# Kernel optimization log

Hardware: AMD Instinct MI355X
Metric: run time of the kernel (lower is better)

Reference implementation:

```python
import jax, jax.numpy as jnp
import numpy as np

EMBED_DIM = 1024
NUM_HEADS = 16
EFF_HEADS = NUM_HEADS // 2
HEAD_DIM = EMBED_DIM // NUM_HEADS
LAMBDA_INIT = 0.8
B, N = 2, 2048


def setup_inputs() -> dict:
    key = jax.random.key(0)
    ks = jax.random.split(key, 14)
    s = 0.02
    return {
        "x": jax.random.normal(ks[0], (B, N, EMBED_DIM), dtype=jnp.float32),
        "Wq": jax.random.normal(ks[1], (EMBED_DIM, EMBED_DIM), dtype=jnp.float32) * s,
        "bq": jnp.zeros((EMBED_DIM,), dtype=jnp.float32),
        "Wk": jax.random.normal(ks[2], (EMBED_DIM, EMBED_DIM), dtype=jnp.float32) * s,
        "bk": jnp.zeros((EMBED_DIM,), dtype=jnp.float32),
        "Wv": jax.random.normal(ks[3], (EMBED_DIM, EMBED_DIM), dtype=jnp.float32) * s,
        "bv": jnp.zeros((EMBED_DIM,), dtype=jnp.float32),
        "Wp": jax.random.normal(ks[4], (EMBED_DIM, EMBED_DIM), dtype=jnp.float32) * s,
        "bp": jnp.zeros((EMBED_DIM,), dtype=jnp.float32),
        "lambda_q1": jax.random.normal(ks[5], (EFF_HEADS, 1, HEAD_DIM), dtype=jnp.float32) * s,
        "lambda_k1": jax.random.normal(ks[6], (EFF_HEADS, 1, HEAD_DIM), dtype=jnp.float32) * s,
        "lambda_q2": jax.random.normal(ks[7], (EFF_HEADS, 1, HEAD_DIM), dtype=jnp.float32) * s,
        "lambda_k2": jax.random.normal(ks[8], (EFF_HEADS, 1, HEAD_DIM), dtype=jnp.float32) * s,
    }


def reference(x, Wq, bq, Wk, bk, Wv, bv, Wp, bp,
              lambda_q1, lambda_k1, lambda_q2, lambda_k2):
    Bb, Nn, C = x.shape
    H, H2, hd = NUM_HEADS, EFF_HEADS, HEAD_DIM
    scale = hd ** (-0.5)

    # projections (torch Linear: y = x @ W.T + b), reshape to [B,H,N,hd]
    q = (x @ Wq.T + bq).reshape(Bb, Nn, H, hd).transpose(0, 2, 1, 3)
    k = (x @ Wk.T + bk).reshape(Bb, Nn, H, hd).transpose(0, 2, 1, 3)
    v = (x @ Wv.T + bv).reshape(Bb, Nn, H, hd).transpose(0, 2, 1, 3)

    q1, q2 = q[:, :H2], q[:, H2:]
    k1, k2 = k[:, :H2], k[:, H2:]
    v1, v2 = v[:, :H2], v[:, H2:]

    # scalar lambda: per-head dot products, clamped exp, differenced, averaged
    l1 = jnp.exp(jnp.minimum((lambda_q1 * lambda_k1).sum((-1, -2)), 5.0))  # [H2]
    l2 = jnp.exp(jnp.minimum((lambda_q2 * lambda_k2).sum((-1, -2)), 5.0))
    lv = (l1 - l2 + LAMBDA_INIT).mean()

    a1 = jax.nn.softmax(jnp.einsum('bhnd,bhmd->bhnm', q1, k1) * scale, axis=-1)
    x1 = jnp.einsum('bhnm,bhmd->bhnd', a1, v1).transpose(0, 2, 1, 3).reshape(Bb, Nn, C // 2)
    a2 = jax.nn.softmax(jnp.einsum('bhnd,bhmd->bhnm', q2, k2) * scale, axis=-1)
    x2 = jnp.einsum('bhnm,bhmd->bhnd', a2, v2).transpose(0, 2, 1, 3).reshape(Bb, Nn, C // 2)

    out = jnp.concatenate([x1 - lv * x2, x2], axis=-1) @ Wp.T + bp
    return out
```

## Files before the change

kernel.cpp:

```cpp
#include <hip/hip_runtime.h>

typedef __bf16 bf16;
typedef __bf16 bf16x8 __attribute__((ext_vector_type(8)));
typedef __bf16 bf16x4 __attribute__((ext_vector_type(4)));
typedef float  f32x16 __attribute__((ext_vector_type(16)));
typedef unsigned int uint;
typedef unsigned int uintx4 __attribute__((ext_vector_type(4)));

#define QSCALE (0.125f * 1.44269504088896340736f)

__device__ __forceinline__ void g2l16(const void* g, void* l) {
  __builtin_amdgcn_global_load_lds(
      (const __attribute__((address_space(1))) void*)g,
      (__attribute__((address_space(3))) void*)l, 16, 0, 0);
}

__device__ __forceinline__ f32x16 mfma16(bf16x8 a, bf16x8 b, f32x16 c) {
  return __builtin_amdgcn_mfma_f32_32x32x16_bf16(a, b, c, 0, 0, 0);
}

__global__ void cast5_kernel(const float* __restrict__ x,
                             const float* __restrict__ wq, const float* __restrict__ wk,
                             const float* __restrict__ wv, const float* __restrict__ wp,
                             const float* __restrict__ lq1, const float* __restrict__ lk1,
                             const float* __restrict__ lq2, const float* __restrict__ lk2,
                             bf16* __restrict__ xb, bf16* __restrict__ wqkv,
                             bf16* __restrict__ wpb) {
  int seg = blockIdx.y;
  long i = (long)(blockIdx.x * 256 + threadIdx.x) * 8;
  const float* s; bf16* d; long n;
  if (seg == 0)      { s = x;  d = xb;  n = 4194304; }
  else if (seg == 1) { s = wq; d = wqkv;            n = 1048576; }
  else if (seg == 2) { s = wk; d = wqkv + 1048576;  n = 1048576; }
  else if (seg == 3) { s = wv; d = wqkv + 2097152;  n = 1048576; }
  else               { s = wp; d = wpb;             n = 1048576; }
  if (i >= n) return;
  float4 f0 = *(const float4*)(s + i);
  float4 f1 = *(const float4*)(s + i + 4);
  if (seg == 4 && (i & 1023) >= 512) {
    int t = threadIdx.x & 63;
    float accum = 0.f;
    for (int hh = 0; hh < 8; ++hh) {
      float v1 = lq1[hh*64 + t] * lk1[hh*64 + t];
      float v2 = lq2[hh*64 + t] * lk2[hh*64 + t];
      for (int off = 32; off; off >>= 1) {
        v1 += __shfl_xor(v1, off);
        v2 += __shfl_xor(v2, off);
      }
      accum += expf(fminf(v1, 5.f)) - expf(fminf(v2, 5.f));
    }
    float lv = accum / 8.f + 0.8f;
    float4 g0 = *(const float4*)(s + i - 512);
    float4 g1 = *(const float4*)(s + i - 508);
    f0.x -= lv * g0.x; f0.y -= lv * g0.y; f0.z -= lv * g0.z; f0.w -= lv * g0.w;
    f1.x -= lv * g1.x; f1.y -= lv * g1.y; f1.z -= lv * g1.z; f1.w -= lv * g1.w;
  }
  bf16x8 o;
  o[0] = (bf16)f0.x; o[1] = (bf16)f0.y; o[2] = (bf16)f0.z; o[3] = (bf16)f0.w;
  o[4] = (bf16)f1.x; o[5] = (bf16)f1.y; o[6] = (bf16)f1.z; o[7] = (bf16)f1.w;
  *(bf16x8*)(d + i) = o;
}

__global__ __launch_bounds__(256, 2) void gemm_qkv_kernel(
    const bf16* __restrict__ A, const bf16* __restrict__ B,
    const float* __restrict__ bias0, const float* __restrict__ bias1,
    const float* __restrict__ bias2,
    bf16* __restrict__ O0, bf16* __restrict__ O1, bf16* __restrict__ O2) {
  __shared__ __align__(16) char smem[32 * 1024];
  const int tid = threadIdx.x;
  const int w = tid >> 6, L = tid & 63;
  const int l31 = L & 31, h5 = L >> 5;
  const int m0 = blockIdx.x * 128;
  const int n0g = blockIdx.y * 128;
  const int by = n0g >> 10;
  const bf16* Bp = B + (long)by * 1048576;
  const float* biasp = (by == 0) ? bias0 : ((by == 1) ? bias1 : bias2);
  const int nloc = n0g & 1023;

  f32x16 acc[2][2];
  for (int i = 0; i < 2; ++i) for (int j = 0; j < 2; ++j)
    for (int r = 0; r < 16; ++r) acc[i][j][r] = 0.f;

  const int srow = L >> 1, spar = L & 1;
  const int wm = w >> 1, wn = w & 1;
  const int fs = (l31 * 2 + h5) * 16;

  for (int k0 = 0; k0 < 1024; k0 += 64) {
    for (int i = 0; i < 8; ++i) {
      int r = w * 8 + i;
      int rr = r & 15;
      int rowblk = rr >> 2, kst = rr & 3;
      int row = rowblk * 32 + srow;
      int kk = k0 + (kst * 2 + spar) * 8;
      const bf16* gsrc = (r < 16) ? (A + (long)(m0 + row) * 1024 + kk)
                                  : (Bp + (long)(nloc + row) * 1024 + kk);
      g2l16(gsrc, smem + r * 1024);
    }
    __syncthreads();
    for (int kst = 0; kst < 4; ++kst) {
      bf16x8 a0 = *(const bf16x8*)(smem + (((wm * 2 + 0) * 4 + kst) * 1024) + fs);
      bf16x8 a1 = *(const bf16x8*)(smem + (((wm * 2 + 1) * 4 + kst) * 1024) + fs);
      bf16x8 b0 = *(const bf16x8*)(smem + 16384 + (((wn * 2 + 0) * 4 + kst) * 1024) + fs);
      bf16x8 b1 = *(const bf16x8*)(smem + 16384 + (((wn * 2 + 1) * 4 + kst) * 1024) + fs);
      acc[0][0] = mfma16(a0, b0, acc[0][0]);
      acc[0][1] = mfma16(a0, b1, acc[0][1]);
      acc[1][0] = mfma16(a1, b0, acc[1][0]);
      acc[1][1] = mfma16(a1, b1, acc[1][1]);
    }
    __syncthreads();
  }

  if (by == 2) {
    int b = m0 >> 11;
    int nbase = (m0 & 2047);
    for (int mi = 0; mi < 2; ++mi) for (int ni = 0; ni < 2; ++ni) {
      int col = nloc + wn * 64 + ni * 32 + l31;
      int hh = col >> 6, d = col & 63;
      float bias_v = biasp[col];
      long rowbase = ((long)(b * 16 + hh) * 64 + d) * 2048 + nbase + wm * 64;
      for (int g = 0; g < 4; ++g) {
        bf16x4 pk;
        for (int r = 0; r < 4; ++r) pk[r] = (bf16)(acc[mi][ni][g * 4 + r] + bias_v);
        int Qp = mi * 4 + g;
        int slot = (Qp >> 1) * 16 + h5 * 8 + (Qp & 1) * 4;
        *(bf16x4*)(O2 + rowbase + slot) = pk;
      }
    }
  } else {
    bf16* dst = (by == 0) ? O0 : O1;
    float scale = (by == 0) ? QSCALE : 1.0f;
    for (int mi = 0; mi < 2; ++mi) for (int ni = 0; ni < 2; ++ni) {
      int col = nloc + wn * 64 + ni * 32 + l31;
      float bias_v = biasp[col];
      int row_base = m0 + wm * 64 + mi * 32 + 4 * h5;
      for (int reg = 0; reg < 16; ++reg) {
        int rowoff = (reg & 3) + 8 * (reg >> 2);
        float v = (acc[mi][ni][reg] + bias_v) * scale;
        dst[(long)(row_base + rowoff) * 1024 + col] = (bf16)v;
      }
    }
  }
}

__global__ __launch_bounds__(256, 2) void gemm_proj_kernel(
    const bf16* __restrict__ A, const bf16* __restrict__ B,
    const float* __restrict__ bias, float* __restrict__ Of) {
  __shared__ __align__(16) char smem[24 * 1024];
  const int tid = threadIdx.x;
  const int w = tid >> 6, L = tid & 63;
  const int l31 = L & 31, h5 = L >> 5;
  const int m0 = blockIdx.x * 64;
  const int nloc = blockIdx.y * 128;

  f32x16 acc[2];
  for (int i = 0; i < 2; ++i)
    for (int r = 0; r < 16; ++r) acc[i][r] = 0.f;

  const int srow = L >> 1, spar = L & 1;
  const int fs = (l31 * 2 + h5) * 16;

  for (int k0 = 0; k0 < 1024; k0 += 64) {
    for (int i = 0; i < 6; ++i) {
      int r = w * 6 + i;
      const bf16* gsrc;
      if (r < 8) {
        int rowblk = r >> 2, kst = r & 3;
        gsrc = A + (long)(m0 + rowblk * 32 + srow) * 1024 + k0 + (kst * 2 + spar) * 8;
      } else {
        int rr = r - 8;
        int rowblk = rr >> 2, kst = rr & 3;
        gsrc = B + (long)(nloc + rowblk * 32 + srow) * 1024 + k0 + (kst * 2 + spar) * 8;
      }
      g2l16(gsrc, smem + r * 1024);
    }
    __syncthreads();
    for (int kst = 0; kst < 4; ++kst) {
      bf16x8 a0 = *(const bf16x8*)(smem + ((0 * 4 + kst) * 1024) + fs);
      bf16x8 a1 = *(const bf16x8*)(smem + ((1 * 4 + kst) * 1024) + fs);
      bf16x8 bb = *(const bf16x8*)(smem + 8192 + ((w * 4 + kst) * 1024) + fs);
      acc[0] = mfma16(a0, bb, acc[0]);
      acc[1] = mfma16(a1, bb, acc[1]);
    }
    __syncthreads();
  }

  for (int mi = 0; mi < 2; ++mi) {
    int col = nloc + w * 32 + l31;
    float bias_v = bias[col];
    int row_base = m0 + mi * 32 + 4 * h5;
    for (int reg = 0; reg < 16; ++reg) {
      int rowoff = (reg & 3) + 8 * (reg >> 2);
      Of[(long)(row_base + rowoff) * 1024 + col] = acc[mi][reg] + bias_v;
    }
  }
}

__global__ __launch_bounds__(512, 4) void attn_kernel(
    const bf16* __restrict__ Qb, const bf16* __restrict__ Kb,
    const bf16* __restrict__ Vt, bf16* __restrict__ Ob) {
  __shared__ __align__(16) char smem[65536];
  const int tid = threadIdx.x, w = tid >> 6, L = tid & 63;
  const int half = w >> 2, pair = w & 3;
  const int bh = blockIdx.x, qt = blockIdx.y;
  const int b = bh >> 4, h = bh & 15;
  const int q0 = qt * 128 + pair * 32;
  const int l31 = L & 31, h5 = L >> 5;
  const int srow = L >> 1, spar = L & 1;
  const int fs = (l31 * 2 + h5) * 16;

  bf16x8 qf[4];
  for (int kst = 0; kst < 4; ++kst)
    qf[kst] = *(const bf16x8*)(Qb + (long)(b * 2048 + q0 + l31) * 1024 + h * 64
                               + kst * 16 + h5 * 8);

  f32x16 o[2];
  for (int i = 0; i < 2; ++i)
    for (int r = 0; r < 16; ++r) o[i][r] = 0.f;
  float ls[4] = {0.f, 0.f, 0.f, 0.f};

  const bf16* Kbh = Kb + (long)b * 2048 * 1024 + h * 64 + (long)half * 1024 * 1024;
  const bf16* Vth = Vt + (long)bh * 64 * 2048 + half * 1024;

  char* kb0 = smem + half * 16384;
  char* kb1 = smem + 32768 + half * 16384;

  auto stage = [&](int t, char* kb) {
    int n0 = t * 64;
    for (int i = 0; i < 4; ++i) {
      int r = pair * 4 + i;
      if (r < 8) {
        int nkb = r >> 2, kst = r & 3;
        const bf16* g = Kbh + (long)(n0 + nkb * 32 + srow) * 1024 + (kst * 2 + spar) * 8;
        g2l16(g, kb + r * 1024);
      } else {
        int rr = r - 8, db = rr >> 2, kst = rr & 3;
        const bf16* g = Vth + (long)(db * 32 + srow) * 2048 + n0 + (kst * 2 + spar) * 8;
        g2l16(g, kb + 8192 + rr * 1024);
      }
    }
  };

  stage(0, kb0);
  stage(1, kb1);

  for (int t = 0; t < 16; ++t) {
    char* kb = (t & 1) ? kb1 : kb0;
    if (t < 15) asm volatile("s_waitcnt vmcnt(4)" ::: "memory");
    else        asm volatile("s_waitcnt vmcnt(0)" ::: "memory");
    __builtin_amdgcn_s_barrier();

    f32x16 s[2];
    {
      bf16x8 k0f = *(const bf16x8*)(kb + fs);
      bf16x8 k1f = *(const bf16x8*)(kb + 4 * 1024 + fs);
      f32x16 z = {};
      __builtin_amdgcn_s_setprio(1);
      s[0] = mfma16(k0f, qf[0], z);
      s[1] = mfma16(k1f, qf[0], z);
      __builtin_amdgcn_s_setprio(0);
    }
    for (int kst = 1; kst < 4; ++kst) {
      bf16x8 k0f = *(const bf16x8*)(kb + (kst * 1024) + fs);
      bf16x8 k1f = *(const bf16x8*)(kb + ((4 + kst) * 1024) + fs);
      __builtin_amdgcn_s_setprio(1);
      s[0] = mfma16(k0f, qf[kst], s[0]);
      s[1] = mfma16(k1f, qf[kst], s[1]);
      __builtin_amdgcn_s_setprio(0);
    }

    for (int nki = 0; nki < 2; ++nki)
      for (int r = 0; r < 16; ++r) {
        float p = __builtin_amdgcn_exp2f(s[nki][r]);
        s[nki][r] = p;
        ls[r & 3] += p;
      }

    for (int kst = 0; kst < 4; ++kst) {
      bf16x8 v0 = *(const bf16x8*)(kb + 8192 + (kst * 1024) + fs);
      bf16x8 v1 = *(const bf16x8*)(kb + 8192 + ((4 + kst) * 1024) + fs);
      int nki = kst >> 1;
      int rbase = (kst & 1) * 8;
      bf16x8 pf;
#pragma unroll
      for (int j = 0; j < 8; ++j) pf[j] = (bf16)s[nki][rbase + j];
      __builtin_amdgcn_s_setprio(1);
      o[0] = mfma16(v0, pf, o[0]);
      o[1] = mfma16(v1, pf, o[1]);
      __builtin_amdgcn_s_setprio(0);
    }

    __builtin_amdgcn_s_barrier();
    if (t + 2 < 16) stage(t + 2, kb);
  }

  float lsum = (ls[0] + ls[1]) + (ls[2] + ls[3]);
  float lcol = lsum + __shfl_xor(lsum, 32);
  if (half) {
    float* dstO = (float*)smem + pair * 2112;
    for (int di = 0; di < 2; ++di)
      for (int r = 0; r < 16; ++r) dstO[L * 33 + di * 16 + r] = o[di][r];
    if (h5 == 0) ((float*)(smem + 33792))[pair * 32 + l31] = lcol;
  }
  __syncthreads();
  float linv = 0.f;
  if (!half) {
    float* srcO = (float*)smem + pair * 2112;
    for (int di = 0; di < 2; ++di)
      for (int r = 0; r < 16; ++r) o[di][r] += srcO[L * 33 + di * 16 + r];
    float lother = ((float*)(smem + 33792))[pair * 32 + l31];
    linv = 1.f / (lcol + lother);
  }
  __syncthreads();
  if (!half) {
    char* ot = smem + pair * 4352;
    for (int di = 0; di < 2; ++di)
      for (int g = 0; g < 4; ++g) {
        bf16x4 pk;
        for (int r = 0; r < 4; ++r)
          pk[r] = (bf16)(o[di][g * 4 + r] * linv);
        int d0 = di * 32 + g * 8 + h5 * 4;
        *(bf16x4*)(ot + (l31 * 68 + d0) * 2) = pk;
      }
    for (int i = 0; i < 4; ++i) {
      int qloc = (L >> 3) + i * 8;
      int cc = L & 7;
      bf16x8 vv = *(const bf16x8*)(ot + (qloc * 68 + cc * 8) * 2);
      *(bf16x8*)(Ob + (long)(b * 2048 + q0 + qloc) * 1024 + h * 64 + cc * 8) = vv;
    }
  }
}

extern "C" void kernel_launch(void* const* d_in, const int* in_sizes, int n_in,
                              void* d_out, int out_size, void* d_ws, size_t ws_size,
                              hipStream_t stream) {
  const float* x   = (const float*)d_in[0];
  const float* Wq  = (const float*)d_in[1];
  const float* bq  = (const float*)d_in[2];
  const float* Wk  = (const float*)d_in[3];
  const float* bk  = (const float*)d_in[4];
  const float* Wv  = (const float*)d_in[5];
  const float* bv  = (const float*)d_in[6];
  const float* Wp  = (const float*)d_in[7];
  const float* bp  = (const float*)d_in[8];
  const float* lq1 = (const float*)d_in[9];
  const float* lk1 = (const float*)d_in[10];
  const float* lq2 = (const float*)d_in[11];
  const float* lk2 = (const float*)d_in[12];
  float* out = (float*)d_out;

  char* ws = (char*)d_ws;
  bf16* xb   = (bf16*)(ws + 1024);
  bf16* Wqkv = xb + (long)4096 * 1024;
  bf16* Wpb  = Wqkv + (long)3 * 1024 * 1024;
  bf16* Vt   = Wpb + (long)1024 * 1024;
  bf16* Ob   = Vt + (long)4096 * 1024;
  bf16* Qb = (bf16*)d_out;
  bf16* Kb = Qb + (long)4096 * 1024;

  cast5_kernel<<<dim3(2048, 5), 256, 0, stream>>>(
      x, Wq, Wk, Wv, Wp, lq1, lk1, lq2, lk2, xb, Wqkv, Wpb);
  gemm_qkv_kernel<<<dim3(32, 24), 256, 0, stream>>>(
      xb, Wqkv, bq, bk, bv, Qb, Kb, Vt);
  attn_kernel<<<dim3(32, 16), 512, 0, stream>>>(Qb, Kb, Vt, Ob);
  gemm_proj_kernel<<<dim3(64, 8), 256, 0, stream>>>(Ob, Wpb, bp, out);
}
```

Baseline: 203.5 us.

## Load V fragments directly from global into registers, shrink LDS to K only

V tiles are no longer staged through LDS. Each lane now reads its V fragments straight from global memory into registers at the start of each iteration, and only K is double-buffered in shared memory. LDS use shrinks from 64KB to about 34KB and the launch bound changes to 2 blocks per SM. The aim is to cut LDS traffic and staging instructions, at the cost of uncoalesced per-lane global loads for V and higher register pressure. The barrier placement also moves: one barrier now comes after QK and another before the epilogue.

Result: slower. 250.3 us (+23.0%).

```diff
diff --git a/kernel.cpp b/kernel.cpp
--- a/kernel.cpp
+++ b/kernel.cpp
@@ -195,10 +195,10 @@
   }
 }
 
-__global__ __launch_bounds__(512, 4) void attn_kernel(
+__global__ __launch_bounds__(512, 2) void attn_kernel(
     const bf16* __restrict__ Qb, const bf16* __restrict__ Kb,
     const bf16* __restrict__ Vt, bf16* __restrict__ Ob) {
-  __shared__ __align__(16) char smem[65536];
+  __shared__ __align__(16) char smem[34816];
   const int tid = threadIdx.x, w = tid >> 6, L = tid & 63;
   const int half = w >> 2, pair = w & 3;
   const int bh = blockIdx.x, qt = blockIdx.y;
@@ -220,34 +220,37 @@
 
   const bf16* Kbh = Kb + (long)b * 2048 * 1024 + h * 64 + (long)half * 1024 * 1024;
   const bf16* Vth = Vt + (long)bh * 64 * 2048 + half * 1024;
-
-  char* kb0 = smem + half * 16384;
-  char* kb1 = smem + 32768 + half * 16384;
-
-  auto stage = [&](int t, char* kb) {
+  const bf16* Vl = Vth + (long)l31 * 2048 + h5 * 8;
+
+  char* kb0 = smem + half * 8192;
+  char* kb1 = smem + 16384 + half * 8192;
+
+  auto stageK = [&](int t, char* kb) {
     int n0 = t * 64;
-    for (int i = 0; i < 4; ++i) {
-      int r = pair * 4 + i;
-      if (r < 8) {
-        int nkb = r >> 2, kst = r & 3;
-        const bf16* g = Kbh + (long)(n0 + nkb * 32 + srow) * 1024 + (kst * 2 + spar) * 8;
-        g2l16(g, kb + r * 1024);
-      } else {
-        int rr = r - 8, db = rr >> 2, kst = rr & 3;
-        const bf16* g = Vth + (long)(db * 32 + srow) * 2048 + n0 + (kst * 2 + spar) * 8;
-        g2l16(g, kb + 8192 + rr * 1024);
-      }
+    for (int i = 0; i < 2; ++i) {
+      int r = pair * 2 + i;
+      int nkb = r >> 2, kst = r & 3;
+      const bf16* g = Kbh + (long)(n0 + nkb * 32 + srow) * 1024 + (kst * 2 + spar) * 8;
+      g2l16(g, kb + r * 1024);
     }
   };
 
-  stage(0, kb0);
-  stage(1, kb1);
+  stageK(0, kb0);
+  stageK(1, kb1);
 
   for (int t = 0; t < 16; ++t) {
     char* kb = (t & 1) ? kb1 : kb0;
-    if (t < 15) asm volatile("s_waitcnt vmcnt(4)" ::: "memory");
-    else        asm volatile("s_waitcnt vmcnt(0)" ::: "memory");
+    asm volatile("s_waitcnt vmcnt(2)" ::: "memory");
     __builtin_amdgcn_s_barrier();
+
+    const int n0 = t * 64;
+
+    bf16x8 v[8];
+#pragma unroll
+    for (int kst = 0; kst < 4; ++kst) {
+      v[kst]     = *(const bf16x8*)(Vl + n0 + kst * 16);
+      v[4 + kst] = *(const bf16x8*)(Vl + 65536 + n0 + kst * 16);
+    }
 
     f32x16 s[2];
     {
@@ -268,6 +271,8 @@
       __builtin_amdgcn_s_setprio(0);
     }
 
+    __builtin_amdgcn_s_barrier();
+
     for (int nki = 0; nki < 2; ++nki)
       for (int r = 0; r < 16; ++r) {
         float p = __builtin_amdgcn_exp2f(s[nki][r]);
@@ -276,25 +281,23 @@
       }
 
     for (int kst = 0; kst < 4; ++kst) {
-      bf16x8 v0 = *(const bf16x8*)(kb + 8192 + (kst * 1024) + fs);
-      bf16x8 v1 = *(const bf16x8*)(kb + 8192 + ((4 + kst) * 1024) + fs);
       int nki = kst >> 1;
       int rbase = (kst & 1) * 8;
       bf16x8 pf;
 #pragma unroll
       for (int j = 0; j < 8; ++j) pf[j] = (bf16)s[nki][rbase + j];
       __builtin_amdgcn_s_setprio(1);
-      o[0] = mfma16(v0, pf, o[0]);
-      o[1] = mfma16(v1, pf, o[1]);
+      o[0] = mfma16(v[kst], pf, o[0]);
+      o[1] = mfma16(v[4 + kst], pf, o[1]);
       __builtin_amdgcn_s_setprio(0);
     }
 
-    __builtin_amdgcn_s_barrier();
-    if (t + 2 < 16) stage(t + 2, kb);
+    if (t + 2 < 16) stageK(t + 2, kb);
   }
 
   float lsum = (ls[0] + ls[1]) + (ls[2] + ls[3]);
   float lcol = lsum + __shfl_xor(lsum, 32);
+  __builtin_amdgcn_s_barrier();
   if (half) {
     float* dstO = (float*)smem + pair * 2112;
     for (int di = 0; di < 2; ++di)
```
